# Kernel tuning notes

Hardware: AMD Instinct MI355X
Metric: run time of the kernel (lower is better)

Reference implementation:

```python
import jax, jax.numpy as jnp
import numpy as np

GRID_SIZE = 128
FEATURE_SIZE = 16
HIDDEN_SIZE = 64
N_POINTS = 2097152


def setup_inputs() -> dict:
    key = jax.random.key(0)
    ks = jax.random.split(key, 8)
    points = jax.random.uniform(ks[0], (N_POINTS, 3), dtype=jnp.float32)
    grid = jax.random.normal(ks[1], (GRID_SIZE, GRID_SIZE, GRID_SIZE, FEATURE_SIZE), dtype=jnp.float32)
    # torch nn.Linear default init: U(-1/sqrt(fan_in), 1/sqrt(fan_in))
    def linear(k, fan_in, fan_out):
        kw, kb = jax.random.split(k)
        bound = 1.0 / np.sqrt(fan_in)
        W = jax.random.uniform(kw, (fan_out, fan_in), minval=-bound, maxval=bound, dtype=jnp.float32)
        b = jax.random.uniform(kb, (fan_out,), minval=-bound, maxval=bound, dtype=jnp.float32)
        return W, b
    W1, b1 = linear(ks[2], FEATURE_SIZE, HIDDEN_SIZE)
    W2, b2 = linear(ks[3], HIDDEN_SIZE, HIDDEN_SIZE)
    W3, b3 = linear(ks[4], HIDDEN_SIZE, 1)
    return {"points": points, "grid": grid, "W1": W1, "b1": b1,
            "W2": W2, "b2": b2, "W3": W3, "b3": b3}


def reference(points, grid, W1, b1, W2, b2, W3, b3):
    gs = grid.shape[0]
    # nearest-grid-node index: scale to [0, gs-1], clamp, round
    p = jnp.clip(points * (gs - 1), 0.0, gs - 1)
    idx = jnp.round(p).astype(jnp.int32)  # (N, 3)
    feats = grid[idx[:, 0], idx[:, 1], idx[:, 2]]  # (N, F) gather
    h = jax.nn.relu(feats @ W1.T + b1)
    h = jax.nn.relu(h @ W2.T + b2)
    occ = jnp.tanh(h @ W3.T + b3)  # (N, 1)
    return occ
```

## Files before the change

### kernel.cpp

```cpp
#include <hip/hip_runtime.h>
#include <hip/hip_fp16.h>
#include <cstdint>
#include <cstddef>


typedef _Float16 half8 __attribute__((ext_vector_type(8)));
typedef float float4v __attribute__((ext_vector_type(4)));

#define WPB 4
#define NT  16

__device__ inline uint32_t pack_f16x2(float a, float b) {
    union { _Float16 h[2]; uint32_t u; } v;
    v.h[0] = (_Float16)a;
    v.h[1] = (_Float16)b;
    return v.u;
}

__global__ __launch_bounds__(256, 3) void occ_mlp_kernel(
    const float* __restrict__ pts,
    const float* __restrict__ grid,
    const float* __restrict__ W1, const float* __restrict__ b1,
    const float* __restrict__ W2, const float* __restrict__ b2,
    const float* __restrict__ W3, const float* __restrict__ b3,
    float* __restrict__ out, int nPoints)
{
    const int lane = threadIdx.x & 63;
    const int l15  = lane & 15;
    const int quad = lane >> 4;
    const int wib  = threadIdx.x >> 6;
    const int tile0 = (blockIdx.x * WPB + wib) * NT;
    const int nTiles = (nPoints + 15) >> 4;
    if (tile0 >= nTiles) return;
    const int maxP = nPoints - 1;

    half8 A1[4];
#pragma unroll
    for (int t = 0; t < 4; ++t) {
        half8 f = {};
        if (quad < 2) {
            const float* row = W1 + (16 * t + l15) * 16 + quad * 8;
#pragma unroll
            for (int j = 0; j < 8; ++j) f[j] = (_Float16)row[j];
        } else if (quad == 2) {
            f[0] = (_Float16)b1[16 * t + l15];
        }
        A1[t] = f;
    }
    half8 A2[4][2];
#pragma unroll
    for (int t = 0; t < 4; ++t)
#pragma unroll
        for (int kk = 0; kk < 2; ++kk) {
            const float* row = W2 + (16 * t + l15) * 64 + 32 * kk + 8 * quad;
            half8 f;
#pragma unroll
            for (int j = 0; j < 8; ++j) f[j] = (_Float16)row[j];
            A2[t][kk] = f;
        }
    float4v bias2[4];
    float w3v[4][4];
#pragma unroll
    for (int t = 0; t < 4; ++t)
#pragma unroll
        for (int r = 0; r < 4; ++r) {
            int h = 16 * t + 4 * quad + r;
            bias2[t][r] = b2[h];
            w3v[t][r]   = W3[h];
        }
    const float bias3 = b3[0];

    const int src0 = l15 + 16 * ((2 * quad) & 3);
    const int src1 = l15 + 16 * ((2 * quad + 1) & 3);
    const bool sel = (quad >> 1) != 0;

    float Px[3], Py[3], Pz[3];
    float4 Fa[2], Fb[2];

    auto loadPts = [&](int slot, int u) {
        int p = (tile0 + u) * 16 + l15;
        p = p > maxP ? maxP : p;
        const float* q = pts + 3 * p;
        Px[slot] = q[0]; Py[slot] = q[1]; Pz[slot] = q[2];
    };
    auto loadFeat = [&](int fslot, int pslot) {
        if (quad < 2) {
            const int ix = (int)rintf(fminf(fmaxf(Px[pslot] * 127.0f, 0.0f), 127.0f));
            const int iy = (int)rintf(fminf(fmaxf(Py[pslot] * 127.0f, 0.0f), 127.0f));
            const int iz = (int)rintf(fminf(fmaxf(Pz[pslot] * 127.0f, 0.0f), 127.0f));
            const int ofs = ((((ix << 7) | iy) << 7) | iz) << 4;
            const float4* g = reinterpret_cast<const float4*>(grid + ofs + (quad << 3));
            Fa[fslot] = g[0];
            Fb[fslot] = g[1];
        }
    };

    loadPts(0, 0); loadPts(1, 1); loadPts(2, 2);
    loadFeat(0, 0);
    loadFeat(1, 1);

    float o[4];

#pragma unroll
    for (int u = 0; u < NT; ++u) {
        half8 bfrag = {};
        if (quad < 2) {
            const float4 f0 = Fa[u & 1];
            const float4 f1 = Fb[u & 1];
            bfrag[0] = (_Float16)f0.x; bfrag[1] = (_Float16)f0.y;
            bfrag[2] = (_Float16)f0.z; bfrag[3] = (_Float16)f0.w;
            bfrag[4] = (_Float16)f1.x; bfrag[5] = (_Float16)f1.y;
            bfrag[6] = (_Float16)f1.z; bfrag[7] = (_Float16)f1.w;
        } else if (quad == 2) {
            bfrag[0] = (_Float16)1.0f;
        }

        if (u + 2 < NT) loadFeat(u & 1, (u + 2) % 3);
        if (u + 3 < NT) loadPts(u % 3, u + 3);

        float4v C1[4];
#pragma unroll
        for (int t = 0; t < 4; ++t) {
            float4v zacc = {};
            C1[t] = __builtin_amdgcn_mfma_f32_16x16x32_f16(A1[t], bfrag, zacc, 0, 0, 0);
        }

        uint32_t P[4][2];
#pragma unroll
        for (int t = 0; t < 4; ++t) {
            P[t][0] = pack_f16x2(fmaxf(C1[t][0], 0.0f), fmaxf(C1[t][1], 0.0f));
            P[t][1] = pack_f16x2(fmaxf(C1[t][2], 0.0f), fmaxf(C1[t][3], 0.0f));
        }

        union Frag { uint32_t u[4]; half8 h; } B2[2];
#pragma unroll
        for (int kk = 0; kk < 2; ++kk) {
            const uint32_t x0a = (uint32_t)__shfl((int)P[2 * kk    ][0], src0);
            const uint32_t x0b = (uint32_t)__shfl((int)P[2 * kk + 1][0], src0);
            const uint32_t x1a = (uint32_t)__shfl((int)P[2 * kk    ][1], src0);
            const uint32_t x1b = (uint32_t)__shfl((int)P[2 * kk + 1][1], src0);
            const uint32_t y0a = (uint32_t)__shfl((int)P[2 * kk    ][0], src1);
            const uint32_t y0b = (uint32_t)__shfl((int)P[2 * kk + 1][0], src1);
            const uint32_t y1a = (uint32_t)__shfl((int)P[2 * kk    ][1], src1);
            const uint32_t y1b = (uint32_t)__shfl((int)P[2 * kk + 1][1], src1);
            B2[kk].u[0] = sel ? x0b : x0a;
            B2[kk].u[1] = sel ? x1b : x1a;
            B2[kk].u[2] = sel ? y0b : y0a;
            B2[kk].u[3] = sel ? y1b : y1a;
        }

        float4v C2[4];
#pragma unroll
        for (int t = 0; t < 4; ++t) C2[t] = bias2[t];
#pragma unroll
        for (int kk = 0; kk < 2; ++kk)
#pragma unroll
            for (int t = 0; t < 4; ++t)
                C2[t] = __builtin_amdgcn_mfma_f32_16x16x32_f16(A2[t][kk], B2[kk].h, C2[t], 0, 0, 0);

        float z = 0.0f;
#pragma unroll
        for (int t = 0; t < 4; ++t)
#pragma unroll
            for (int r = 0; r < 4; ++r)
                z = fmaf(fmaxf(C2[t][r], 0.0f), w3v[t][r], z);
        z += __shfl_xor(z, 16);
        z += __shfl_xor(z, 32);
        const float e = __expf(2.0f * (z + bias3));
        o[u & 3] = fmaf(-2.0f, __builtin_amdgcn_rcpf(e + 1.0f), 1.0f);

        if ((u & 3) == 3) {
            const float osel = (quad == 0) ? o[0] : (quad == 1) ? o[1]
                             : (quad == 2) ? o[2] : o[3];
            const int pstore = (tile0 + (u & ~3)) * 16 + lane;
            if (pstore <= maxP) out[pstore] = osel;
        }

        asm volatile("" ::: "memory");
    }
}

extern "C" void kernel_launch(void* const* d_in, const int* in_sizes, int n_in,
                              void* d_out, int out_size, void* d_ws, size_t ws_size,
                              hipStream_t stream)
{
    const float* pts  = (const float*)d_in[0];
    const float* grid = (const float*)d_in[1];
    const float* W1   = (const float*)d_in[2];
    const float* b1   = (const float*)d_in[3];
    const float* W2   = (const float*)d_in[4];
    const float* b2   = (const float*)d_in[5];
    const float* W3   = (const float*)d_in[6];
    const float* b3   = (const float*)d_in[7];
    float* out = (float*)d_out;
    const int nPoints = in_sizes[0] / 3;

    const int nTiles = (nPoints + 15) >> 4;
    const int tilesPerBlock = WPB * NT;
    const int nBlocks = (nTiles + tilesPerBlock - 1) / tilesPerBlock;

    occ_mlp_kernel<<<dim3(nBlocks), dim3(256), 0, stream>>>(
        pts, grid, W1, b1, W2, b2, W3, b3, out, nPoints);
}
```

Baseline: 272.7 us.

## Gather features for two tiles per wave using all lanes and deepen prefetch

Previously only half the lanes (quads 0-1) issued grid gathers, one 16-point tile at a time. Now all four quads gather, covering two tiles per load round: quads 0-1 take the first tile and quads 2-3 the second. The second tile's features are moved into position with cross-lane shuffles (xor 32). The prefetch pipeline is deepened to three feature slots ahead, aiming to raise memory-level parallelism and hide gather latency, at the cost of extra registers and shuffle instructions.

```diff
diff --git a/kernel.cpp b/kernel.cpp
--- a/kernel.cpp
+++ b/kernel.cpp
@@ -9,6 +9,7 @@
 
 #define WPB 4
 #define NT  16
+#define NP  8
 
 __device__ inline uint32_t pack_f16x2(float a, float b) {
     union { _Float16 h[2]; uint32_t u; } v;
@@ -33,6 +34,10 @@
     const int nTiles = (nPoints + 15) >> 4;
     if (tile0 >= nTiles) return;
     const int maxP = nPoints - 1;
+    const int pt0  = tile0 << 4;
+
+    const int half = quad & 1;
+    const int tsel = quad >> 1;
 
     half8 A1[4];
 #pragma unroll
@@ -74,106 +79,122 @@
     const int src1 = l15 + 16 * ((2 * quad + 1) & 3);
     const bool sel = (quad >> 1) != 0;
 
-    float Px[3], Py[3], Pz[3];
-    float4 Fa[2], Fb[2];
-
-    auto loadPts = [&](int slot, int u) {
-        int p = (tile0 + u) * 16 + l15;
+    float Cx[3], Cy[3], Cz[3];
+    float4 Fa[4], Fb[4];
+
+    auto loadCoords = [&](int slot, int v) {
+        int p = pt0 + v * 32 + (tsel << 4) + l15;
         p = p > maxP ? maxP : p;
         const float* q = pts + 3 * p;
-        Px[slot] = q[0]; Py[slot] = q[1]; Pz[slot] = q[2];
+        Cx[slot] = q[0]; Cy[slot] = q[1]; Cz[slot] = q[2];
     };
-    auto loadFeat = [&](int fslot, int pslot) {
-        if (quad < 2) {
-            const int ix = (int)rintf(fminf(fmaxf(Px[pslot] * 127.0f, 0.0f), 127.0f));
-            const int iy = (int)rintf(fminf(fmaxf(Py[pslot] * 127.0f, 0.0f), 127.0f));
-            const int iz = (int)rintf(fminf(fmaxf(Pz[pslot] * 127.0f, 0.0f), 127.0f));
-            const int ofs = ((((ix << 7) | iy) << 7) | iz) << 4;
-            const float4* g = reinterpret_cast<const float4*>(grid + ofs + (quad << 3));
-            Fa[fslot] = g[0];
-            Fb[fslot] = g[1];
-        }
+    auto loadFeat = [&](int fslot, int cslot) {
+        const int ix = (int)rintf(fminf(fmaxf(Cx[cslot] * 127.0f, 0.0f), 127.0f));
+        const int iy = (int)rintf(fminf(fmaxf(Cy[cslot] * 127.0f, 0.0f), 127.0f));
+        const int iz = (int)rintf(fminf(fmaxf(Cz[cslot] * 127.0f, 0.0f), 127.0f));
+        const int ofs = ((((ix << 7) | iy) << 7) | iz) << 4;
+        const float4* g = reinterpret_cast<const float4*>(grid + ofs + (half << 3));
+        Fa[fslot] = g[0];
+        Fb[fslot] = g[1];
     };
 
-    loadPts(0, 0); loadPts(1, 1); loadPts(2, 2);
-    loadFeat(0, 0);
-    loadFeat(1, 1);
+    loadCoords(0, 0); loadCoords(1, 1); loadCoords(2, 2);
+    loadFeat(0, 0); loadFeat(1, 1); loadFeat(2, 2);
+    loadCoords(0, 3); loadCoords(1, 4);
 
     float o[4];
 
 #pragma unroll
-    for (int u = 0; u < NT; ++u) {
-        half8 bfrag = {};
-        if (quad < 2) {
-            const float4 f0 = Fa[u & 1];
-            const float4 f1 = Fb[u & 1];
-            bfrag[0] = (_Float16)f0.x; bfrag[1] = (_Float16)f0.y;
-            bfrag[2] = (_Float16)f0.z; bfrag[3] = (_Float16)f0.w;
-            bfrag[4] = (_Float16)f1.x; bfrag[5] = (_Float16)f1.y;
-            bfrag[6] = (_Float16)f1.z; bfrag[7] = (_Float16)f1.w;
-        } else if (quad == 2) {
-            bfrag[0] = (_Float16)1.0f;
-        }
-
-        if (u + 2 < NT) loadFeat(u & 1, (u + 2) % 3);
-        if (u + 3 < NT) loadPts(u % 3, u + 3);
-
-        float4v C1[4];
-#pragma unroll
-        for (int t = 0; t < 4; ++t) {
-            float4v zacc = {};
-            C1[t] = __builtin_amdgcn_mfma_f32_16x16x32_f16(A1[t], bfrag, zacc, 0, 0, 0);
-        }
-
-        uint32_t P[4][2];
-#pragma unroll
-        for (int t = 0; t < 4; ++t) {
-            P[t][0] = pack_f16x2(fmaxf(C1[t][0], 0.0f), fmaxf(C1[t][1], 0.0f));
-            P[t][1] = pack_f16x2(fmaxf(C1[t][2], 0.0f), fmaxf(C1[t][3], 0.0f));
-        }
-
-        union Frag { uint32_t u[4]; half8 h; } B2[2];
-#pragma unroll
-        for (int kk = 0; kk < 2; ++kk) {
-            const uint32_t x0a = (uint32_t)__shfl((int)P[2 * kk    ][0], src0);
-            const uint32_t x0b = (uint32_t)__shfl((int)P[2 * kk + 1][0], src0);
-            const uint32_t x1a = (uint32_t)__shfl((int)P[2 * kk    ][1], src0);
-            const uint32_t x1b = (uint32_t)__shfl((int)P[2 * kk + 1][1], src0);
-            const uint32_t y0a = (uint32_t)__shfl((int)P[2 * kk    ][0], src1);
-            const uint32_t y0b = (uint32_t)__shfl((int)P[2 * kk + 1][0], src1);
-            const uint32_t y1a = (uint32_t)__shfl((int)P[2 * kk    ][1], src1);
-            const uint32_t y1b = (uint32_t)__shfl((int)P[2 * kk + 1][1], src1);
-            B2[kk].u[0] = sel ? x0b : x0a;
-            B2[kk].u[1] = sel ? x1b : x1a;
-            B2[kk].u[2] = sel ? y0b : y0a;
-            B2[kk].u[3] = sel ? y1b : y1a;
-        }
-
-        float4v C2[4];
-#pragma unroll
-        for (int t = 0; t < 4; ++t) C2[t] = bias2[t];
-#pragma unroll
-        for (int kk = 0; kk < 2; ++kk)
+    for (int v = 0; v < NP; ++v) {
+        const int s = v & 3;
+
+#pragma unroll
+        for (int tt = 0; tt < 2; ++tt) {
+            const int u = 2 * v + tt;
+
+            float4 f0, f1;
+            if (tt == 0) {
+                f0 = Fa[s];
+                f1 = Fb[s];
+            } else {
+                f0.x = __shfl_xor(Fa[s].x, 32); f0.y = __shfl_xor(Fa[s].y, 32);
+                f0.z = __shfl_xor(Fa[s].z, 32); f0.w = __shfl_xor(Fa[s].w, 32);
+                f1.x = __shfl_xor(Fb[s].x, 32); f1.y = __shfl_xor(Fb[s].y, 32);
+                f1.z = __shfl_xor(Fb[s].z, 32); f1.w = __shfl_xor(Fb[s].w, 32);
+            }
+
+            half8 bfrag = {};
+            if (quad < 2) {
+                bfrag[0] = (_Float16)f0.x; bfrag[1] = (_Float16)f0.y;
+                bfrag[2] = (_Float16)f0.z; bfrag[3] = (_Float16)f0.w;
+                bfrag[4] = (_Float16)f1.x; bfrag[5] = (_Float16)f1.y;
+                bfrag[6] = (_Float16)f1.z; bfrag[7] = (_Float16)f1.w;
+            } else if (quad == 2) {
+                bfrag[0] = (_Float16)1.0f;
+            }
+
+            if (tt == 0) {
+                if (v + 3 < NP) loadFeat((v + 3) & 3, v % 3);
+                if (v + 5 < NP) loadCoords((v + 2) % 3, v + 5);
+            }
+
+            float4v C1[4];
+#pragma unroll
+            for (int t = 0; t < 4; ++t) {
+                float4v zacc = {};
+                C1[t] = __builtin_amdgcn_mfma_f32_16x16x32_f16(A1[t], bfrag, zacc, 0, 0, 0);
+            }
+
+            uint32_t P[4][2];
+#pragma unroll
+            for (int t = 0; t < 4; ++t) {
+                P[t][0] = pack_f16x2(fmaxf(C1[t][0], 0.0f), fmaxf(C1[t][1], 0.0f));
+                P[t][1] = pack_f16x2(fmaxf(C1[t][2], 0.0f), fmaxf(C1[t][3], 0.0f));
+            }
+
+            union Frag { uint32_t u[4]; half8 h; } B2[2];
+#pragma unroll
+            for (int kk = 0; kk < 2; ++kk) {
+                const uint32_t x0a = (uint32_t)__shfl((int)P[2 * kk    ][0], src0);
+                const uint32_t x0b = (uint32_t)__shfl((int)P[2 * kk + 1][0], src0);
+                const uint32_t x1a = (uint32_t)__shfl((int)P[2 * kk    ][1], src0);
+                const uint32_t x1b = (uint32_t)__shfl((int)P[2 * kk + 1][1], src0);
+                const uint32_t y0a = (uint32_t)__shfl((int)P[2 * kk    ][0], src1);
+                const uint32_t y0b = (uint32_t)__shfl((int)P[2 * kk + 1][0], src1);
+                const uint32_t y1a = (uint32_t)__shfl((int)P[2 * kk    ][1], src1);
+                const uint32_t y1b = (uint32_t)__shfl((int)P[2 * kk + 1][1], src1);
+                B2[kk].u[0] = sel ? x0b : x0a;
+                B2[kk].u[1] = sel ? x1b : x1a;
+                B2[kk].u[2] = sel ? y0b : y0a;
+                B2[kk].u[3] = sel ? y1b : y1a;
+            }
+
+            float4v C2[4];
+#pragma unroll
+            for (int t = 0; t < 4; ++t) C2[t] = bias2[t];
+#pragma unroll
+            for (int kk = 0; kk < 2; ++kk)
+#pragma unroll
+                for (int t = 0; t < 4; ++t)
+                    C2[t] = __builtin_amdgcn_mfma_f32_16x16x32_f16(A2[t][kk], B2[kk].h, C2[t], 0, 0, 0);
+
+            float z = 0.0f;
 #pragma unroll
             for (int t = 0; t < 4; ++t)
-                C2[t] = __builtin_amdgcn_mfma_f32_16x16x32_f16(A2[t][kk], B2[kk].h, C2[t], 0, 0, 0);
-
-        float z = 0.0f;
-#pragma unroll
-        for (int t = 0; t < 4; ++t)
-#pragma unroll
-            for (int r = 0; r < 4; ++r)
-                z = fmaf(fmaxf(C2[t][r], 0.0f), w3v[t][r], z);
-        z += __shfl_xor(z, 16);
-        z += __shfl_xor(z, 32);
-        const float e = __expf(2.0f * (z + bias3));
-        o[u & 3] = fmaf(-2.0f, __builtin_amdgcn_rcpf(e + 1.0f), 1.0f);
-
-        if ((u & 3) == 3) {
-            const float osel = (quad == 0) ? o[0] : (quad == 1) ? o[1]
-                             : (quad == 2) ? o[2] : o[3];
-            const int pstore = (tile0 + (u & ~3)) * 16 + lane;
-            if (pstore <= maxP) out[pstore] = osel;
+#pragma unroll
+                for (int r = 0; r < 4; ++r)
+                    z = fmaf(fmaxf(C2[t][r], 0.0f), w3v[t][r], z);
+            z += __shfl_xor(z, 16);
+            z += __shfl_xor(z, 32);
+            const float e = __expf(2.0f * (z + bias3));
+            o[u & 3] = fmaf(-2.0f, __builtin_amdgcn_rcpf(e + 1.0f), 1.0f);
+
+            if ((u & 3) == 3) {
+                const float osel = (quad == 0) ? o[0] : (quad == 1) ? o[1]
+                                 : (quad == 2) ? o[2] : o[3];
+                const int pstore = (tile0 + (u & ~3)) * 16 + lane;
+                if (pstore <= maxP) out[pstore] = osel;
+            }
         }
 
         asm volatile("" ::: "memory");
```

Measured after the change: 249.7 us. 1.09x faster.
